# Optimization experiments

Measured on AMD Instinct MI355X. Metric: run time of the kernel, lower is better.

Reference implementation:

```python
import jax, jax.numpy as jnp
import numpy as np

N = 50000      # nodes
D = 128        # input_dim == hidden_dim (required by aggrmethod='add')
E_ADJ = 800000 # nonzeros in sparse adjacency
E_PRED = 500000
L = 2          # nbaselayer
BN_EPS = 1e-5


def setup_inputs() -> dict:
    key = jax.random.key(0)
    ks = jax.random.split(key, 10)
    x = jax.random.normal(ks[0], (N, D), dtype=jnp.float32)
    adj_row = jax.random.randint(ks[1], (E_ADJ,), 0, N, dtype=jnp.int32)
    adj_col = jax.random.randint(ks[2], (E_ADJ,), 0, N, dtype=jnp.int32)
    # positive values ~ normalized adjacency weights (avg degree 16)
    adj_val = jax.random.uniform(ks[3], (E_ADJ,), dtype=jnp.float32) / 16.0
    edge_index = jax.random.randint(ks[4], (2, E_PRED), 0, N, dtype=jnp.int32)
    s = 1.0 / np.sqrt(D).astype(np.float32)
    W = jax.random.uniform(ks[5], (L, D, D), jnp.float32, -s, s)
    W_self = jax.random.uniform(ks[6], (L, D, D), jnp.float32, -s, s)
    b = jax.random.uniform(ks[7], (L, D), jnp.float32, -s, s)
    gamma = jnp.ones((L, D), jnp.float32)
    beta = jnp.zeros((L, D), jnp.float32)
    sc = 1.0 / np.sqrt(2 * D).astype(np.float32)
    Wc = jax.random.uniform(ks[8], (2 * D, 1), jnp.float32, -sc, sc)
    bc = jax.random.uniform(ks[9], (1,), jnp.float32, -sc, sc)
    return dict(x=x, adj_row=adj_row, adj_col=adj_col, adj_val=adj_val,
                edge_index=edge_index, W=W, W_self=W_self, b=b,
                gamma=gamma, beta=beta, Wc=Wc, bc=bc)


def _batchnorm(h, g, be):
    # BatchNorm1d over node dim, training-mode (batch) statistics, biased var
    mu = jnp.mean(h, axis=0)
    var = jnp.mean(jnp.square(h - mu), axis=0)
    return g * (h - mu) * jax.lax.rsqrt(var + BN_EPS) + be


def reference(x, adj_row, adj_col, adj_val, edge_index, W, W_self, b, gamma, beta, Wc, bc):
    h = x
    for i in range(L):  # GraphConvolutionBS layers
        support = h @ W[i]                                  # [N, D]
        # spmm(adj, support): gather by col, scale by val, scatter-add by row
        agg = jax.ops.segment_sum(adj_val[:, None] * support[adj_col],
                                  adj_row, num_segments=N)   # [N, D]
        out = agg + h @ W_self[i] + b[i]                    # self-loop + bias
        h = jax.nn.relu(_batchnorm(out, gamma[i], beta[i]))
        # dropout omitted (eval mode)
    node_emb = h + x  # aggrmethod='add', dense=False: residual with block input
    emb1 = node_emb[edge_index[0]]                          # [E_PRED, D]
    emb2 = node_emb[edge_index[1]]
    edge_emb = jnp.concatenate([emb1, emb2], axis=1)        # [E_PRED, 2D]
    return jax.nn.sigmoid(edge_emb @ Wc + bc)               # [E_PRED, 1]
```

## Files before the change

### kernel.cpp

```cpp
#include <hip/hip_runtime.h>
#include <hip/hip_bf16.h>
#include <hip/hip_fp16.h>

#define DD 128
#define BN_EPS 1e-5f
#define SPMM_BLOCKS 2048
#define CAP 64
#define OVF_MAX 4096

typedef __attribute__((ext_vector_type(8))) short bf16x8;
typedef __attribute__((ext_vector_type(4))) float f32x4;

static __device__ __forceinline__ unsigned short f2bf(float f) {
    __hip_bfloat16 h = __float2bfloat16(f);
    return *reinterpret_cast<unsigned short*>(&h);
}
static __device__ __forceinline__ float bf2f(unsigned short u) {
    return __uint_as_float(((unsigned)u) << 16);
}
static __device__ __forceinline__ unsigned pack_rec(int col, float val) {
    __half h = __float2half(val);
    unsigned hb = *reinterpret_cast<unsigned short*>(&h);
    return (unsigned)col | (hb << 16);
}
static __device__ __forceinline__ float rec_val(unsigned rec) {
    unsigned short hb = (unsigned short)(rec >> 16);
    __half h = *reinterpret_cast<__half*>(&hb);
    return __half2float(h);
}

__global__ __launch_bounds__(256) void prep_zero(
    const float* __restrict__ W, const float* __restrict__ Wself,
    unsigned short* __restrict__ Wt4, int* __restrict__ zp, int nz)
{
    if (blockIdx.x < 32) {
        int mat   = blockIdx.x >> 3;
        int chunk = blockIdx.x & 7;
        int layer = mat >> 1;
        const float* src = (mat & 1) ? (Wself + layer * 16384) : (W + layer * 16384);
        unsigned short* dst = Wt4 + (size_t)mat * 16384;
        int base = chunk * 2048 + threadIdx.x * 4;
        #pragma unroll
        for (int rep = 0; rep < 2; rep++) {
            int i = base + rep * 1024;
            float4 v = *(const float4*)&src[i];
            int k = i >> 7, n = i & 127;
            dst[(n + 0) * 128 + k] = f2bf(v.x);
            dst[(n + 1) * 128 + k] = f2bf(v.y);
            dst[(n + 2) * 128 + k] = f2bf(v.z);
            dst[(n + 3) * 128 + k] = f2bf(v.w);
        }
    } else {
        int i = (blockIdx.x - 32) * 256 + threadIdx.x;
        if (i < nz) zp[i] = 0;
    }
}

__global__ __launch_bounds__(1024) void scatter_bucket(
    const int* __restrict__ arow, const int* __restrict__ acol,
    const float* __restrict__ aval, int* __restrict__ cnt,
    unsigned* __restrict__ bucket, int* __restrict__ ovfc,
    int2* __restrict__ ovf, int E, int rpp)
{
    const int p     = blockIdx.x & 7;
    const int slice = blockIdx.x >> 3;
    const int nsl   = gridDim.x >> 3;
    const int e0    = (int)((long long)E * slice / nsl);
    const int e1    = (int)((long long)E * (slice + 1) / nsl);
    for (int e = e0 + threadIdx.x; e < e1; e += 1024) {
        int r = arow[e];
        if (r / rpp == p) {
            int pos = atomicAdd(&cnt[r], 1);
            unsigned rec = pack_rec(acol[e], aval[e]);
            if (pos < CAP) {
                __builtin_nontemporal_store(rec, &bucket[(size_t)r * CAP + pos]);
            } else {
                int oi = atomicAdd(ovfc, 1);
                if (oi < OVF_MAX) ovf[oi] = make_int2(r, (int)rec);
            }
        }
    }
}

__global__ __launch_bounds__(256) void gemm_mfma(
    const float* __restrict__ A,
    const unsigned short* __restrict__ Wt, const unsigned short* __restrict__ Wst,
    const float* __restrict__ bias,
    const float* __restrict__ stats, const float* __restrict__ gamma,
    const float* __restrict__ beta, float invN, int useBN,
    unsigned short* __restrict__ support, float* __restrict__ outb, int N)
{
    __shared__ float ssc[128], ssh[128];
    if (useBN) {
        if (threadIdx.x < 128) {
            int c = threadIdx.x;
            float mean = stats[c] * invN;
            float var  = stats[128 + c] * invN - mean * mean;
            float sc   = gamma[c] * rsqrtf(var + BN_EPS);
            ssc[c] = sc;
            ssh[c] = beta[c] - mean * sc;
        }
        __syncthreads();
    }

    const int wave = threadIdx.x >> 6;
    const int lane = threadIdx.x & 63;
    const int m    = lane & 15;
    const int quad = lane >> 4;
    const int row0 = blockIdx.x * 64 + wave * 16;

    int arow = row0 + m; if (arow > N - 1) arow = N - 1;
    const float* Ar = A + (size_t)arow * 128;
    bf16x8 af[4];
    #pragma unroll
    for (int ch = 0; ch < 4; ch++) {
        int k0 = ch * 32 + quad * 8;
        float4 u = *(const float4*)&Ar[k0];
        float4 v = *(const float4*)&Ar[k0 + 4];
        float vals[8] = {u.x, u.y, u.z, u.w, v.x, v.y, v.z, v.w};
        #pragma unroll
        for (int j = 0; j < 8; j++) {
            float val = vals[j];
            if (useBN) {
                val = val * ssc[k0 + j] + ssh[k0 + j];
                val = val > 0.f ? val : 0.f;
            }
            af[ch][j] = (short)f2bf(val);
        }
    }

    f32x4 acc1[8], acc2[8];
    #pragma unroll
    for (int nt = 0; nt < 8; nt++) {
        acc1[nt] = (f32x4)(0.f);
        acc2[nt] = (f32x4)(0.f);
    }

    #pragma unroll
    for (int nt = 0; nt < 8; nt++) {
        const bf16x8* B1 = (const bf16x8*)(Wt  + ((size_t)(nt * 16 + m)) * 128 + quad * 8);
        const bf16x8* B2 = (const bf16x8*)(Wst + ((size_t)(nt * 16 + m)) * 128 + quad * 8);
        acc1[nt] = __builtin_amdgcn_mfma_f32_16x16x32_bf16(af[0], B1[0],  acc1[nt], 0, 0, 0);
        acc2[nt] = __builtin_amdgcn_mfma_f32_16x16x32_bf16(af[0], B2[0],  acc2[nt], 0, 0, 0);
        acc1[nt] = __builtin_amdgcn_mfma_f32_16x16x32_bf16(af[1], B1[4],  acc1[nt], 0, 0, 0);
        acc2[nt] = __builtin_amdgcn_mfma_f32_16x16x32_bf16(af[1], B2[4],  acc2[nt], 0, 0, 0);
        acc1[nt] = __builtin_amdgcn_mfma_f32_16x16x32_bf16(af[2], B1[8],  acc1[nt], 0, 0, 0);
        acc2[nt] = __builtin_amdgcn_mfma_f32_16x16x32_bf16(af[2], B2[8],  acc2[nt], 0, 0, 0);
        acc1[nt] = __builtin_amdgcn_mfma_f32_16x16x32_bf16(af[3], B1[12], acc1[nt], 0, 0, 0);
        acc2[nt] = __builtin_amdgcn_mfma_f32_16x16x32_bf16(af[3], B2[12], acc2[nt], 0, 0, 0);
    }

    float bv[8];
    #pragma unroll
    for (int nt = 0; nt < 8; nt++) bv[nt] = bias[nt * 16 + m];

    #pragma unroll
    for (int r = 0; r < 4; r++) {
        int orow = row0 + quad * 4 + r;
        if (orow < N) {
            size_t base = (size_t)orow * 128 + m;
            #pragma unroll
            for (int nt = 0; nt < 8; nt++) {
                support[base + nt * 16] = f2bf(acc1[nt][r]);
                outb[base + nt * 16]    = acc2[nt][r] + bv[nt];
            }
        }
    }
}

__global__ __launch_bounds__(256) void spmm_stats(
    const int* __restrict__ cnt, const unsigned* __restrict__ bucket,
    const int* __restrict__ ovfc, const int2* __restrict__ ovf,
    const unsigned short* __restrict__ sup, float* __restrict__ outb,
    float* __restrict__ partials, int ngroups, int N)
{
    const int r    = threadIdx.x & 31;
    const int slot = threadIdx.x >> 5;
    float s4[4] = {0.f, 0.f, 0.f, 0.f};
    float q4[4] = {0.f, 0.f, 0.f, 0.f};

    for (int g = blockIdx.x; g < ngroups; g += gridDim.x) {
        int row = g * 8 + slot;
        if (row >= N) continue;
        int nrec = cnt[row]; if (nrec > CAP) nrec = CAP;
        const unsigned* packed = bucket + (size_t)row * CAP;

        float4 acc = make_float4(0.f, 0.f, 0.f, 0.f);
        int e = 0;
        for (; e + 4 <= nrec; e += 4) {
            unsigned p0 = packed[e + 0];
            unsigned p1 = packed[e + 1];
            unsigned p2 = packed[e + 2];
            unsigned p3 = packed[e + 3];
            ushort4 s0 = *(const ushort4*)&sup[((size_t)(p0 & 0xFFFFu) << 7) + r * 4];
            ushort4 s1 = *(const ushort4*)&sup[((size_t)(p1 & 0xFFFFu) << 7) + r * 4];
            ushort4 s2 = *(const ushort4*)&sup[((size_t)(p2 & 0xFFFFu) << 7) + r * 4];
            ushort4 s3 = *(const ushort4*)&sup[((size_t)(p3 & 0xFFFFu) << 7) + r * 4];
            float v0 = rec_val(p0), v1 = rec_val(p1);
            float v2 = rec_val(p2), v3 = rec_val(p3);
            acc.x += v0 * bf2f(s0.x); acc.y += v0 * bf2f(s0.y);
            acc.z += v0 * bf2f(s0.z); acc.w += v0 * bf2f(s0.w);
            acc.x += v1 * bf2f(s1.x); acc.y += v1 * bf2f(s1.y);
            acc.z += v1 * bf2f(s1.z); acc.w += v1 * bf2f(s1.w);
            acc.x += v2 * bf2f(s2.x); acc.y += v2 * bf2f(s2.y);
            acc.z += v2 * bf2f(s2.z); acc.w += v2 * bf2f(s2.w);
            acc.x += v3 * bf2f(s3.x); acc.y += v3 * bf2f(s3.y);
            acc.z += v3 * bf2f(s3.z); acc.w += v3 * bf2f(s3.w);
        }
        for (; e < nrec; e++) {
            unsigned pr = packed[e];
            ushort4 sv = *(const ushort4*)&sup[((size_t)(pr & 0xFFFFu) << 7) + r * 4];
            float v = rec_val(pr);
            acc.x += v * bf2f(sv.x); acc.y += v * bf2f(sv.y);
            acc.z += v * bf2f(sv.z); acc.w += v * bf2f(sv.w);
        }

        int oc = *ovfc;
        if (oc > 0) {
            if (oc > OVF_MAX) oc = OVF_MAX;
            for (int i = 0; i < oc; i++) {
                int2 orec = ovf[i];
                if (orec.x == row) {
                    unsigned pr = (unsigned)orec.y;
                    ushort4 sv = *(const ushort4*)&sup[((size_t)(pr & 0xFFFFu) << 7) + r * 4];
                    float v = rec_val(pr);
                    acc.x += v * bf2f(sv.x); acc.y += v * bf2f(sv.y);
                    acc.z += v * bf2f(sv.z); acc.w += v * bf2f(sv.w);
                }
            }
        }

        float4* op = (float4*)&outb[((size_t)row << 7) + r * 4];
        float4 o = *op;
        o.x += acc.x; o.y += acc.y; o.z += acc.z; o.w += acc.w;
        *op = o;
        s4[0] += o.x; s4[1] += o.y; s4[2] += o.z; s4[3] += o.w;
        q4[0] += o.x * o.x; q4[1] += o.y * o.y; q4[2] += o.z * o.z; q4[3] += o.w * o.w;
    }

    __shared__ float red[8][128];
    #pragma unroll
    for (int j = 0; j < 4; j++) red[slot][r * 4 + j] = s4[j];
    __syncthreads();
    float ts = 0.f;
    if (threadIdx.x < 128) {
        #pragma unroll
        for (int j = 0; j < 8; j++) ts += red[j][threadIdx.x];
        partials[(size_t)blockIdx.x * 256 + threadIdx.x] = ts;
    }
    __syncthreads();
    #pragma unroll
    for (int j = 0; j < 4; j++) red[slot][r * 4 + j] = q4[j];
    __syncthreads();
    if (threadIdx.x < 128) {
        float tq = 0.f;
        #pragma unroll
        for (int j = 0; j < 8; j++) tq += red[j][threadIdx.x];
        partials[(size_t)blockIdx.x * 256 + 128 + threadIdx.x] = tq;
    }
}

__global__ __launch_bounds__(256) void reduce_stats(
    const float* __restrict__ partials, float* __restrict__ stats, int nblk)
{
    int g = blockIdx.x;
    int per = (nblk + gridDim.x - 1) / gridDim.x;
    int b0 = g * per, b1 = min(b0 + per, nblk);
    float a0 = 0.f;
    for (int b = b0; b < b1; b++) {
        a0 += partials[(size_t)b * 256 + threadIdx.x];
    }
    atomicAdd(&stats[threadIdx.x], a0);
}

__global__ __launch_bounds__(256) void score_kernel(
    const float* __restrict__ outb, const float* __restrict__ stats,
    const float* __restrict__ gamma, const float* __restrict__ beta,
    const float* __restrict__ x, const float* __restrict__ Wc,
    float* __restrict__ s1, float* __restrict__ s2, float invN, int N)
{
    int idx = blockIdx.x * 256 + threadIdx.x;
    if (idx >= N * 32) return;
    int c4 = (idx & 31) * 4;
    float4 o = *(const float4*)&outb[(size_t)idx * 4];
    float res[4];
    const float* op = &o.x;
    #pragma unroll
    for (int j = 0; j < 4; j++) {
        int c = c4 + j;
        float mean = stats[c] * invN;
        float var  = stats[128 + c] * invN - mean * mean;
        float sc   = gamma[c] * rsqrtf(var + BN_EPS);
        float sh   = beta[c] - mean * sc;
        float v    = op[j] * sc + sh;
        res[j] = v > 0.f ? v : 0.f;
    }
    float4 xv = *(const float4*)&x[(size_t)idx * 4];
    res[0] += xv.x; res[1] += xv.y; res[2] += xv.z; res[3] += xv.w;
    float4 w1 = *(const float4*)&Wc[c4];
    float4 w2 = *(const float4*)&Wc[128 + c4];
    float a1 = res[0] * w1.x + res[1] * w1.y + res[2] * w1.z + res[3] * w1.w;
    float a2 = res[0] * w2.x + res[1] * w2.y + res[2] * w2.z + res[3] * w2.w;
    #pragma unroll
    for (int off = 1; off < 32; off <<= 1) {
        a1 += __shfl_xor(a1, off);
        a2 += __shfl_xor(a2, off);
    }
    if ((idx & 31) == 0) {
        int row = idx >> 5;
        s1[row] = a1;
        s2[row] = a2;
    }
}

__global__ __launch_bounds__(256) void edge_pred_scalar(
    const float* __restrict__ s1, const float* __restrict__ s2,
    const int* __restrict__ ei, const float* __restrict__ bc,
    float* __restrict__ outp, int Ep)
{
    int e = blockIdx.x * 256 + threadIdx.x;
    if (e >= Ep) return;
    float v = s1[ei[e]] + s2[ei[Ep + e]] + bc[0];
    outp[e] = 1.f / (1.f + expf(-v));
}

extern "C" void kernel_launch(void* const* d_in, const int* in_sizes, int n_in,
                              void* d_out, int out_size, void* d_ws, size_t ws_size,
                              hipStream_t stream) {
    const float* x        = (const float*)d_in[0];
    const int*   adj_row  = (const int*)  d_in[1];
    const int*   adj_col  = (const int*)  d_in[2];
    const float* adj_val  = (const float*)d_in[3];
    const int*   ei       = (const int*)  d_in[4];
    const float* W        = (const float*)d_in[5];
    const float* W_self   = (const float*)d_in[6];
    const float* b        = (const float*)d_in[7];
    const float* gamma    = (const float*)d_in[8];
    const float* beta     = (const float*)d_in[9];
    const float* Wc       = (const float*)d_in[10];
    const float* bc       = (const float*)d_in[11];
    float* outp = (float*)d_out;

    const int N  = in_sizes[0] / DD;
    const int E  = in_sizes[1];
    const int Ep = in_sizes[4] / 2;
    const float invN = 1.f / (float)N;

    size_t nd = (size_t)N * DD;
    char* p = (char*)d_ws;
    unsigned short* support16 = (unsigned short*)p; p += nd * 2;
    float*          outbA     = (float*)p;          p += nd * 4;
    float*          outbB     = (float*)p;          p += nd * 4;
    unsigned short* Wt4       = (unsigned short*)p; p += 4 * 16384 * 2;
    float*          stats     = (float*)p;          p += 512 * 4;
    int*            cnt       = (int*)p;            p += (size_t)N * 4;
    int*            ovfc      = (int*)p;            p += 4;
    unsigned*       bucket    = (unsigned*)p;       p += (size_t)N * CAP * 4;
    int2*           ovf       = (int2*)p;           p += (size_t)OVF_MAX * 8;
    float*          s1        = (float*)p;          p += (size_t)N * 4;
    float*          s2        = (float*)p;          p += (size_t)N * 4;
    float*          partials  = (float*)p;          p += (size_t)SPMM_BLOCKS * 256 * 4;

    const int rpp = (N + 7) / 8;
    const int ngroups = (N + 7) / 8;
    const int nz = 512 + N + 1;

    prep_zero<<<32 + (nz + 255) / 256, 256, 0, stream>>>(W, W_self, Wt4, (int*)stats, nz);
    scatter_bucket<<<256, 1024, 0, stream>>>(
        adj_row, adj_col, adj_val, cnt, bucket, ovfc, ovf, E, rpp);

    const int gemm_grid  = (N + 63) / 64;
    const int score_grid = (N * 32 + 255) / 256;

    gemm_mfma<<<gemm_grid, 256, 0, stream>>>(
        x, Wt4 + 0 * 16384, Wt4 + 1 * 16384, b,
        nullptr, nullptr, nullptr, invN, 0,
        support16, outbA, N);
    spmm_stats<<<SPMM_BLOCKS, 256, 0, stream>>>(
        cnt, bucket, ovfc, ovf, support16, outbA, partials, ngroups, N);
    reduce_stats<<<32, 256, 0, stream>>>(partials, stats, SPMM_BLOCKS);

    gemm_mfma<<<gemm_grid, 256, 0, stream>>>(
        outbA, Wt4 + 2 * 16384, Wt4 + 3 * 16384, b + DD,
        stats, gamma, beta, invN, 1,
        support16, outbB, N);
    spmm_stats<<<SPMM_BLOCKS, 256, 0, stream>>>(
        cnt, bucket, ovfc, ovf, support16, outbB, partials, ngroups, N);
    reduce_stats<<<32, 256, 0, stream>>>(partials, stats + 256, SPMM_BLOCKS);

    score_kernel<<<score_grid, 256, 0, stream>>>(
        outbB, stats + 256, gamma + DD, beta + DD, x, Wc, s1, s2, invN, N);
    edge_pred_scalar<<<(Ep + 255) / 256, 256, 0, stream>>>(s1, s2, ei, bc, outp, Ep);
}
```

Before: 332.8 us.

## Fuse adjacency bucket scatter into layer-0 GEMM launch and halve bucket capacity

Merges the edge-bucketing scatter kernel into the first-layer GEMM launch, so that extra blocks do the scatter while the GEMM blocks run. This removes one kernel launch and lets the two independent stages overlap. The bucket capacity per row is halved and the overflow list enlarged, shrinking the bucket array and its footprint in spmm. The nontemporal store is replaced by a plain store, and the GEMM is split into a non-BN and a BN variant so the BN branch no longer sits behind a runtime flag. The cost is that more edges take the slower overflow path, and with average degree 16 some rows will exceed 32 entries.

```diff
diff --git a/kernel.cpp b/kernel.cpp
--- a/kernel.cpp
+++ b/kernel.cpp
@@ -5,8 +5,9 @@
 #define DD 128
 #define BN_EPS 1e-5f
 #define SPMM_BLOCKS 2048
-#define CAP 64
-#define OVF_MAX 4096
+#define SCAT_BLOCKS 2048
+#define CAP 32
+#define OVF_MAX 8192
 
 typedef __attribute__((ext_vector_type(8))) short bf16x8;
 typedef __attribute__((ext_vector_type(4))) float f32x4;
@@ -56,24 +57,23 @@
     }
 }
 
-__global__ __launch_bounds__(1024) void scatter_bucket(
+static __device__ __forceinline__ void scatter_body(
+    int j, int nsl, int p,
     const int* __restrict__ arow, const int* __restrict__ acol,
     const float* __restrict__ aval, int* __restrict__ cnt,
     unsigned* __restrict__ bucket, int* __restrict__ ovfc,
-    int2* __restrict__ ovf, int E, int rpp)
-{
-    const int p     = blockIdx.x & 7;
-    const int slice = blockIdx.x >> 3;
-    const int nsl   = gridDim.x >> 3;
-    const int e0    = (int)((long long)E * slice / nsl);
-    const int e1    = (int)((long long)E * (slice + 1) / nsl);
-    for (int e = e0 + threadIdx.x; e < e1; e += 1024) {
+    int2* __restrict__ ovf, int E, int rpp, int tstride)
+{
+    const int slice = j >> 3;
+    const int e0 = (int)((long long)E * slice / nsl);
+    const int e1 = (int)((long long)E * (slice + 1) / nsl);
+    for (int e = e0 + threadIdx.x; e < e1; e += tstride) {
         int r = arow[e];
         if (r / rpp == p) {
             int pos = atomicAdd(&cnt[r], 1);
             unsigned rec = pack_rec(acol[e], aval[e]);
             if (pos < CAP) {
-                __builtin_nontemporal_store(rec, &bucket[(size_t)r * CAP + pos]);
+                bucket[(size_t)r * CAP + pos] = rec;
             } else {
                 int oi = atomicAdd(ovfc, 1);
                 if (oi < OVF_MAX) ovf[oi] = make_int2(r, (int)rec);
@@ -82,25 +82,22 @@
     }
 }
 
-__global__ __launch_bounds__(256) void gemm_mfma(
+__global__ __launch_bounds__(256) void gemm_l0_scatter(
     const float* __restrict__ A,
     const unsigned short* __restrict__ Wt, const unsigned short* __restrict__ Wst,
     const float* __restrict__ bias,
-    const float* __restrict__ stats, const float* __restrict__ gamma,
-    const float* __restrict__ beta, float invN, int useBN,
-    unsigned short* __restrict__ support, float* __restrict__ outb, int N)
-{
-    __shared__ float ssc[128], ssh[128];
-    if (useBN) {
-        if (threadIdx.x < 128) {
-            int c = threadIdx.x;
-            float mean = stats[c] * invN;
-            float var  = stats[128 + c] * invN - mean * mean;
-            float sc   = gamma[c] * rsqrtf(var + BN_EPS);
-            ssc[c] = sc;
-            ssh[c] = beta[c] - mean * sc;
-        }
-        __syncthreads();
+    unsigned short* __restrict__ support, float* __restrict__ outb, int N, int gemm_grid,
+    const int* __restrict__ arow, const int* __restrict__ acol,
+    const float* __restrict__ aval, int* __restrict__ cnt,
+    unsigned* __restrict__ bucket, int* __restrict__ ovfc,
+    int2* __restrict__ ovf, int E, int rpp)
+{
+    if (blockIdx.x >= gemm_grid) {
+        int j   = blockIdx.x - gemm_grid;
+        int nsl = (gridDim.x - gemm_grid) >> 3;
+        int p   = blockIdx.x & 7;
+        scatter_body(j, nsl, p, arow, acol, aval, cnt, bucket, ovfc, ovf, E, rpp, 256);
+        return;
     }
 
     const int wave = threadIdx.x >> 6;
@@ -109,8 +106,82 @@
     const int quad = lane >> 4;
     const int row0 = blockIdx.x * 64 + wave * 16;
 
-    int arow = row0 + m; if (arow > N - 1) arow = N - 1;
-    const float* Ar = A + (size_t)arow * 128;
+    int ar = row0 + m; if (ar > N - 1) ar = N - 1;
+    const float* Ar = A + (size_t)ar * 128;
+    bf16x8 af[4];
+    #pragma unroll
+    for (int ch = 0; ch < 4; ch++) {
+        int k0 = ch * 32 + quad * 8;
+        float4 u = *(const float4*)&Ar[k0];
+        float4 v = *(const float4*)&Ar[k0 + 4];
+        float vals[8] = {u.x, u.y, u.z, u.w, v.x, v.y, v.z, v.w};
+        #pragma unroll
+        for (int jj = 0; jj < 8; jj++) af[ch][jj] = (short)f2bf(vals[jj]);
+    }
+
+    f32x4 acc1[8], acc2[8];
+    #pragma unroll
+    for (int nt = 0; nt < 8; nt++) { acc1[nt] = (f32x4)(0.f); acc2[nt] = (f32x4)(0.f); }
+
+    #pragma unroll
+    for (int nt = 0; nt < 8; nt++) {
+        const bf16x8* B1 = (const bf16x8*)(Wt  + ((size_t)(nt * 16 + m)) * 128 + quad * 8);
+        const bf16x8* B2 = (const bf16x8*)(Wst + ((size_t)(nt * 16 + m)) * 128 + quad * 8);
+        acc1[nt] = __builtin_amdgcn_mfma_f32_16x16x32_bf16(af[0], B1[0],  acc1[nt], 0, 0, 0);
+        acc2[nt] = __builtin_amdgcn_mfma_f32_16x16x32_bf16(af[0], B2[0],  acc2[nt], 0, 0, 0);
+        acc1[nt] = __builtin_amdgcn_mfma_f32_16x16x32_bf16(af[1], B1[4],  acc1[nt], 0, 0, 0);
+        acc2[nt] = __builtin_amdgcn_mfma_f32_16x16x32_bf16(af[1], B2[4],  acc2[nt], 0, 0, 0);
+        acc1[nt] = __builtin_amdgcn_mfma_f32_16x16x32_bf16(af[2], B1[8],  acc1[nt], 0, 0, 0);
+        acc2[nt] = __builtin_amdgcn_mfma_f32_16x16x32_bf16(af[2], B2[8],  acc2[nt], 0, 0, 0);
+        acc1[nt] = __builtin_amdgcn_mfma_f32_16x16x32_bf16(af[3], B1[12], acc1[nt], 0, 0, 0);
+        acc2[nt] = __builtin_amdgcn_mfma_f32_16x16x32_bf16(af[3], B2[12], acc2[nt], 0, 0, 0);
+    }
+
+    float bv[8];
+    #pragma unroll
+    for (int nt = 0; nt < 8; nt++) bv[nt] = bias[nt * 16 + m];
+
+    #pragma unroll
+    for (int r = 0; r < 4; r++) {
+        int orow = row0 + quad * 4 + r;
+        if (orow < N) {
+            size_t base = (size_t)orow * 128 + m;
+            #pragma unroll
+            for (int nt = 0; nt < 8; nt++) {
+                support[base + nt * 16] = f2bf(acc1[nt][r]);
+                outb[base + nt * 16]    = acc2[nt][r] + bv[nt];
+            }
+        }
+    }
+}
+
+__global__ __launch_bounds__(256) void gemm_mfma_bn(
+    const float* __restrict__ A,
+    const unsigned short* __restrict__ Wt, const unsigned short* __restrict__ Wst,
+    const float* __restrict__ bias,
+    const float* __restrict__ stats, const float* __restrict__ gamma,
+    const float* __restrict__ beta, float invN,
+    unsigned short* __restrict__ support, float* __restrict__ outb, int N)
+{
+    __shared__ float ssc[128], ssh[128];
+    if (threadIdx.x < 128) {
+        int c = threadIdx.x;
+        float mean = stats[c] * invN;
+        float var  = stats[128 + c] * invN - mean * mean;
+        float sc   = gamma[c] * rsqrtf(var + BN_EPS);
+        ssc[c] = sc;
+        ssh[c] = beta[c] - mean * sc;
+    }
+    __syncthreads();
+
+    const int wave = threadIdx.x >> 6;
+    const int lane = threadIdx.x & 63;
+    const int m    = lane & 15;
+    const int quad = lane >> 4;
+    const int row0 = blockIdx.x * 64 + wave * 16;
+
+    int ar = row0 + m; if (ar > N - 1) ar = N - 1;
+    const float* Ar = A + (size_t)ar * 128;
     bf16x8 af[4];
     #pragma unroll
     for (int ch = 0; ch < 4; ch++) {
@@ -120,21 +191,15 @@
         float vals[8] = {u.x, u.y, u.z, u.w, v.x, v.y, v.z, v.w};
         #pragma unroll
         for (int j = 0; j < 8; j++) {
-            float val = vals[j];
-            if (useBN) {
-                val = val * ssc[k0 + j] + ssh[k0 + j];
-                val = val > 0.f ? val : 0.f;
-            }
+            float val = vals[j] * ssc[k0 + j] + ssh[k0 + j];
+            val = val > 0.f ? val : 0.f;
             af[ch][j] = (short)f2bf(val);
         }
     }
 
     f32x4 acc1[8], acc2[8];
     #pragma unroll
-    for (int nt = 0; nt < 8; nt++) {
-        acc1[nt] = (f32x4)(0.f);
-        acc2[nt] = (f32x4)(0.f);
-    }
+    for (int nt = 0; nt < 8; nt++) { acc1[nt] = (f32x4)(0.f); acc2[nt] = (f32x4)(0.f); }
 
     #pragma unroll
     for (int nt = 0; nt < 8; nt++) {
@@ -365,24 +430,22 @@
     const int ngroups = (N + 7) / 8;
     const int nz = 512 + N + 1;
 
-    prep_zero<<<32 + (nz + 255) / 256, 256, 0, stream>>>(W, W_self, Wt4, (int*)stats, nz);
-    scatter_bucket<<<256, 1024, 0, stream>>>(
-        adj_row, adj_col, adj_val, cnt, bucket, ovfc, ovf, E, rpp);
-
     const int gemm_grid  = (N + 63) / 64;
     const int score_grid = (N * 32 + 255) / 256;
 
-    gemm_mfma<<<gemm_grid, 256, 0, stream>>>(
+    prep_zero<<<32 + (nz + 255) / 256, 256, 0, stream>>>(W, W_self, Wt4, (int*)stats, nz);
+
+    gemm_l0_scatter<<<gemm_grid + SCAT_BLOCKS, 256, 0, stream>>>(
         x, Wt4 + 0 * 16384, Wt4 + 1 * 16384, b,
-        nullptr, nullptr, nullptr, invN, 0,
-        support16, outbA, N);
+        support16, outbA, N, gemm_grid,
+        adj_row, adj_col, adj_val, cnt, bucket, ovfc, ovf, E, rpp);
     spmm_stats<<<SPMM_BLOCKS, 256, 0, stream>>>(
         cnt, bucket, ovfc, ovf, support16, outbA, partials, ngroups, N);
     reduce_stats<<<32, 256, 0, stream>>>(partials, stats, SPMM_BLOCKS);
 
-    gemm_mfma<<<gemm_grid, 256, 0, stream>>>(
+    gemm_mfma_bn<<<gemm_grid, 256, 0, stream>>>(
         outbA, Wt4 + 2 * 16384, Wt4 + 3 * 16384, b + DD,
-        stats, gamma, beta, invN, 1,
+        stats, gamma, beta, invN,
         support16, outbB, N);
     spmm_stats<<<SPMM_BLOCKS, 256, 0, stream>>>(
         cnt, bucket, ovfc, ovf, support16, outbB, partials, ngroups, N);
```

Result: faster. 308.3 us (-7.4%).
